# Optimization experiments

Measured on AMD Instinct MI355X. Metric: run time of the kernel, lower is better.

Reference implementation:

```python
import jax, jax.numpy as jnp
import numpy as np


def setup_inputs() -> dict:
    key = jax.random.key(0)
    k1, k2, k3, k4, k5, k6 = jax.random.split(key, 6)
    B, T, K = 64, 1024, 256
    inputs = jax.random.normal(k1, (B, T, K), dtype=jnp.float32)
    tags = jax.random.randint(k2, (B, T), 0, K, dtype=jnp.int64)
    mask = jnp.ones((B, T), dtype=jnp.int32)
    # xavier_normal-ish std for [K,K]: sqrt(2/(K+K))
    transitions = jax.random.normal(k3, (K, K), dtype=jnp.float32) * np.float32(np.sqrt(1.0 / K))
    start_transitions = jax.random.normal(k4, (K,), dtype=jnp.float32)
    end_transitions = jax.random.normal(k5, (K,), dtype=jnp.float32)
    return {
        "inputs": inputs,
        "tags": tags,
        "mask": mask,
        "transitions": transitions,
        "start_transitions": start_transitions,
        "end_transitions": end_transitions,
    }


def _crf_log_likelihood(inputs, tags, mask, transitions, start_transitions, end_transitions):
    # inputs: [B,T,K] emission logits; tags/mask: [B,T]
    B, T, K = inputs.shape
    logits = jnp.transpose(inputs, (1, 0, 2))      # [T,B,K]
    tags_t = tags.T                                 # [T,B]
    maskf = mask.T.astype(inputs.dtype)             # [T,B]
    lengths = jnp.sum(mask, axis=1)                 # [B]
    end_idx = lengths - 1                           # last valid timestep per batch

    # ---- numerator: score of the gold path ----
    # potentials[t,b,i,j] = logits[t,b,i] + transitions[j,i]; gold path picks
    # (i=tags[t], j=tags[t-1]); t=0 picks column 0 = logits[0]+start.
    emit = jnp.take_along_axis(logits, tags_t[:, :, None], axis=2)[..., 0]  # [T,B]
    trans_sc = transitions[tags_t[:-1], tags_t[1:]]                          # [T-1,B]
    last_tags = tags_t[end_idx, jnp.arange(B)]                               # [B]
    numerator = (emit[0]
                 + start_transitions[tags_t[0]]
                 + jnp.sum(maskf[1:] * (emit[1:] + trans_sc), axis=0)
                 + end_transitions[last_tags])                               # [B]

    # ---- denominator: forward algorithm (log-sum-exp over all paths) ----
    is_end = (jnp.arange(T)[:, None] == end_idx[None, :]).astype(inputs.dtype)  # [T,B]
    alpha0 = logits[0] + start_transitions[None, :] + is_end[0][:, None] * end_transitions[None, :]

    def step(alpha, xs):
        lg, m, ie = xs  # lg: [B,K], m/ie: [B]
        # alpha_new[b,i] = logsumexp_j(alpha[b,j] + transitions[j,i]) + logits[t,b,i]
        new = jax.nn.logsumexp(alpha[:, :, None] + transitions[None, :, :], axis=1)
        new = new + lg + ie[:, None] * end_transitions[None, :]
        alpha = jnp.where(m[:, None] > 0, new, alpha)
        return alpha, None

    alphaT, _ = jax.lax.scan(step, alpha0, (logits[1:], maskf[1:], is_end[1:]))
    denominator = jax.nn.logsumexp(alphaT, axis=1)  # [B]

    return jnp.sum(numerator - denominator)


def reference(inputs, tags, mask, transitions, start_transitions, end_transitions):
    return _crf_log_likelihood(inputs, tags, mask, transitions, start_transitions, end_transitions)
```

## Files before the change

kernel.cpp:

```cpp
#include <hip/hip_runtime.h>
#include <hip/hip_fp16.h>

namespace {
constexpr int Bn = 64;
constexpr int Tn = 1024;
constexpr int Kn = 256;
constexpr int TH = 512;

constexpr float LOG2E  = 1.4426950408889634f;
constexpr float LN2    = 0.6931471805599453f;
constexpr float RBIAS  = 4.0f;
constexpr float PCLAMP = 15.5f;

typedef _Float16 half8 __attribute__((ext_vector_type(8)));
typedef float f32x4 __attribute__((ext_vector_type(4)));

__device__ __forceinline__ float fexp2(float x) {
    float r; asm("v_exp_f32 %0, %1" : "=v"(r) : "v"(x)); return r;
}
__device__ __forceinline__ float flog2(float x) {
    float r; asm("v_log_f32 %0, %1" : "=v"(r) : "v"(x)); return r;
}

template <int C>
__device__ __forceinline__ float dppmax1(float x) {
    int o = __builtin_bit_cast(int, x);
    int y = __builtin_amdgcn_update_dpp(o, o, C, 0xF, 0xF, false);
    return fmaxf(x, __builtin_bit_cast(float, y));
}
template <int C>
__device__ __forceinline__ float dppadd1(float x) {
    int y = __builtin_amdgcn_update_dpp(0, __builtin_bit_cast(int, x), C, 0xF, 0xF, true);
    return x + __builtin_bit_cast(float, y);
}
__device__ __forceinline__ float wave_max64(float x) {
    x = dppmax1<0x111>(x);
    x = dppmax1<0x112>(x);
    x = dppmax1<0x114>(x);
    x = dppmax1<0x118>(x);
    x = dppmax1<0x142>(x);
    x = dppmax1<0x143>(x);
    return __builtin_bit_cast(float,
        __builtin_amdgcn_readlane(__builtin_bit_cast(int, x), 63));
}
__device__ __forceinline__ float wave_sum64(float x) {
    x = dppadd1<0x111>(x);
    x = dppadd1<0x112>(x);
    x = dppadd1<0x114>(x);
    x = dppadd1<0x118>(x);
    x = dppadd1<0x142>(x);
    x = dppadd1<0x143>(x);
    return __builtin_bit_cast(float,
        __builtin_amdgcn_readlane(__builtin_bit_cast(int, x), 63));
}
__device__ __forceinline__ float tree4(const f32x4 m) {
    return fmaxf(fmaxf(m[0], m[1]), fmaxf(m[2], m[3]));
}

__global__ __launch_bounds__(256) void efrag_kernel(
    const float* __restrict__ trans, _Float16* __restrict__ efrag)
{
    const int g   = blockIdx.x * 256 + threadIdx.x;
    const int dir = g >> 13;
    const int gg  = g & 8191;
    const int l   = gg & 63;
    const int kt  = (gg >> 6) & 7;
    const int c   = (gg >> 9) & 3;
    const int wg  = (gg >> 11) & 3;
    const int n   = 64 * wg + 16 * c + (l & 15);
    const int k0  = 32 * kt + (l >> 4) * 8;
    half8 hb;
#pragma unroll
    for (int i = 0; i < 8; ++i) {
        const int k = k0 + i;
        hb[i] = (_Float16)__expf(dir == 0 ? trans[k * Kn + n]
                                          : trans[n * Kn + k]);
    }
    ((half8*)efrag)[g] = hb;
}

#define MFMA32_SELECT()                                                          \
    const half8* prow = (const half8*)(&p_sh[PB][0]);                            \
    half8 af0 = prow[0 * 4 + La], af1 = prow[1 * 4 + La];                        \
    half8 af2 = prow[2 * 4 + La], af3 = prow[3 * 4 + La];                        \
    half8 af4 = prow[4 * 4 + La], af5 = prow[5 * 4 + La];                        \
    half8 af6 = prow[6 * 4 + La], af7 = prow[7 * 4 + La];                        \
    f32x4 a0 = __builtin_amdgcn_mfma_f32_16x16x32_f16(af0, Bfrag[0][0], zacc, 0, 0, 0); \
    f32x4 a1 = __builtin_amdgcn_mfma_f32_16x16x32_f16(af0, Bfrag[1][0], zacc, 0, 0, 0); \
    f32x4 a2 = __builtin_amdgcn_mfma_f32_16x16x32_f16(af0, Bfrag[2][0], zacc, 0, 0, 0); \
    f32x4 a3 = __builtin_amdgcn_mfma_f32_16x16x32_f16(af0, Bfrag[3][0], zacc, 0, 0, 0); \
    a0 = __builtin_amdgcn_mfma_f32_16x16x32_f16(af1, Bfrag[0][1], a0, 0, 0, 0);  \
    a1 = __builtin_amdgcn_mfma_f32_16x16x32_f16(af1, Bfrag[1][1], a1, 0, 0, 0);  \
    a2 = __builtin_amdgcn_mfma_f32_16x16x32_f16(af1, Bfrag[2][1], a2, 0, 0, 0);  \
    a3 = __builtin_amdgcn_mfma_f32_16x16x32_f16(af1, Bfrag[3][1], a3, 0, 0, 0);  \
    a0 = __builtin_amdgcn_mfma_f32_16x16x32_f16(af2, Bfrag[0][2], a0, 0, 0, 0);  \
    a1 = __builtin_amdgcn_mfma_f32_16x16x32_f16(af2, Bfrag[1][2], a1, 0, 0, 0);  \
    a2 = __builtin_amdgcn_mfma_f32_16x16x32_f16(af2, Bfrag[2][2], a2, 0, 0, 0);  \
    a3 = __builtin_amdgcn_mfma_f32_16x16x32_f16(af2, Bfrag[3][2], a3, 0, 0, 0);  \
    a0 = __builtin_amdgcn_mfma_f32_16x16x32_f16(af3, Bfrag[0][3], a0, 0, 0, 0);  \
    a1 = __builtin_amdgcn_mfma_f32_16x16x32_f16(af3, Bfrag[1][3], a1, 0, 0, 0);  \
    a2 = __builtin_amdgcn_mfma_f32_16x16x32_f16(af3, Bfrag[2][3], a2, 0, 0, 0);  \
    a3 = __builtin_amdgcn_mfma_f32_16x16x32_f16(af3, Bfrag[3][3], a3, 0, 0, 0);  \
    a0 = __builtin_amdgcn_mfma_f32_16x16x32_f16(af4, Bfrag[0][4], a0, 0, 0, 0);  \
    a1 = __builtin_amdgcn_mfma_f32_16x16x32_f16(af4, Bfrag[1][4], a1, 0, 0, 0);  \
    a2 = __builtin_amdgcn_mfma_f32_16x16x32_f16(af4, Bfrag[2][4], a2, 0, 0, 0);  \
    a3 = __builtin_amdgcn_mfma_f32_16x16x32_f16(af4, Bfrag[3][4], a3, 0, 0, 0);  \
    a0 = __builtin_amdgcn_mfma_f32_16x16x32_f16(af5, Bfrag[0][5], a0, 0, 0, 0);  \
    a1 = __builtin_amdgcn_mfma_f32_16x16x32_f16(af5, Bfrag[1][5], a1, 0, 0, 0);  \
    a2 = __builtin_amdgcn_mfma_f32_16x16x32_f16(af5, Bfrag[2][5], a2, 0, 0, 0);  \
    a3 = __builtin_amdgcn_mfma_f32_16x16x32_f16(af5, Bfrag[3][5], a3, 0, 0, 0);  \
    a0 = __builtin_amdgcn_mfma_f32_16x16x32_f16(af6, Bfrag[0][6], a0, 0, 0, 0);  \
    a1 = __builtin_amdgcn_mfma_f32_16x16x32_f16(af6, Bfrag[1][6], a1, 0, 0, 0);  \
    a2 = __builtin_amdgcn_mfma_f32_16x16x32_f16(af6, Bfrag[2][6], a2, 0, 0, 0);  \
    a3 = __builtin_amdgcn_mfma_f32_16x16x32_f16(af6, Bfrag[3][6], a3, 0, 0, 0);  \
    a0 = __builtin_amdgcn_mfma_f32_16x16x32_f16(af7, Bfrag[0][7], a0, 0, 0, 0);  \
    a1 = __builtin_amdgcn_mfma_f32_16x16x32_f16(af7, Bfrag[1][7], a1, 0, 0, 0);  \
    a2 = __builtin_amdgcn_mfma_f32_16x16x32_f16(af7, Bfrag[2][7], a2, 0, 0, 0);  \
    a3 = __builtin_amdgcn_mfma_f32_16x16x32_f16(af7, Bfrag[3][7], a3, 0, 0, 0);  \
    const float s01 = (La & 1) ? a1[0] : a0[0];                                  \
    const float s23 = (La & 1) ? a3[0] : a2[0];                                  \
    const float s   = (La & 2) ? s23 : s01;

template <int PB, int NB>
__device__ __forceinline__ void fwd_step(
    int tcur, float& alpha, float& R_prev,
    float& lg1, float& lg2, float& lg3,
    const float* __restrict__ in_b, int j_own, int La, int wg,
    const half8 (&Bfrag)[4][8], const f32x4 zacc,
    _Float16 (*__restrict__ p_sh)[Kn], float (*__restrict__ Mv)[4])
{
    const float lgC = lg1; lg1 = lg2; lg2 = lg3;
    lg3 = in_b[(size_t)(tcur + 3) * Kn + j_own];
    const float early = fmaf(lgC, LOG2E, R_prev);

    asm volatile("s_waitcnt lgkmcnt(0)" ::: "memory");
    __builtin_amdgcn_s_barrier();
    __builtin_amdgcn_sched_barrier(0);

    const f32x4 mv = *(const f32x4*)(&Mv[NB][0]);
    const float wmx = wave_max64(alpha);
    Mv[PB][wg] = wmx;
    const float R_use = tree4(mv) + RBIAS;

    MFMA32_SELECT()

    alpha = early + flog2(s);
    const float pv = fexp2(fminf(alpha - R_use, PCLAMP));
    p_sh[NB][j_own] = (_Float16)pv;
    R_prev = R_use;
}

template <int PB, int NB>
__device__ __forceinline__ void bwd_step(
    int tcur, float& beta, float& x, float& R_prev,
    float& lg1, float& lg2, float& lg3,
    const float* __restrict__ in_b, int j_own, int La, int wg,
    const half8 (&Bfrag)[4][8], const f32x4 zacc,
    _Float16 (*__restrict__ p_sh)[Kn], float (*__restrict__ Mv)[4])
{
    const float lgC = lg1; lg1 = lg2; lg2 = lg3;
    lg3 = in_b[(size_t)(tcur - 3) * Kn + j_own];
    const float lgC2 = lgC * LOG2E;

    asm volatile("s_waitcnt lgkmcnt(0)" ::: "memory");
    __builtin_amdgcn_s_barrier();
    __builtin_amdgcn_sched_barrier(0);

    const f32x4 mv = *(const f32x4*)(&Mv[NB][0]);
    const float wmx = wave_max64(x);
    Mv[PB][wg] = wmx;
    const float R_use = tree4(mv) + RBIAS;

    MFMA32_SELECT()

    beta = R_prev + flog2(s);
    x = beta + lgC2;
    const float qv = fexp2(fminf(x - R_use, PCLAMP));
    p_sh[NB][j_own] = (_Float16)qv;
    R_prev = R_use;
}

template <int PB, int NB>
__device__ __forceinline__ void m_step(
    int tcur, float& alpha, float& R_prev,
    float& lg1, float& lg2, float& lg3,
    const float* __restrict__ in_b, int j_own, int La, int wg,
    const half8 (&Bfrag)[4][8], const f32x4 zacc,
    _Float16 (*__restrict__ p_sh)[Kn], float (*__restrict__ Mv)[4],
    const int* __restrict__ mask_sh)
{
    const float lgC = lg1; lg1 = lg2; lg2 = lg3;
    const int tp3 = (tcur + 3 < Tn) ? (tcur + 3) : (Tn - 1);
    lg3 = in_b[(size_t)tp3 * Kn + j_own];
    const int mkC = mask_sh[tcur];

    asm volatile("s_waitcnt lgkmcnt(0)" ::: "memory");
    __builtin_amdgcn_s_barrier();
    __builtin_amdgcn_sched_barrier(0);

    const f32x4 mv = *(const f32x4*)(&Mv[NB][0]);
    const float wmx = wave_max64(alpha);
    Mv[PB][wg] = wmx;
    const float R_use = tree4(mv) + RBIAS;

    MFMA32_SELECT()

    const float na = R_prev + flog2(s) + lgC * LOG2E;
    if (mkC > 0) alpha = na;
    const float pv = fexp2(fminf(alpha - R_use, PCLAMP));
    p_sh[NB][j_own] = (_Float16)pv;
    R_prev = R_use;
}

__global__ __launch_bounds__(256, 1) void crf_main(
    const float* __restrict__ inputs,
    const long long* __restrict__ tags,
    const int* __restrict__ mask,
    const _Float16* __restrict__ efrag,
    const float* __restrict__ trans,
    const float* __restrict__ start_t,
    const float* __restrict__ end_t,
    float* __restrict__ out,
    float* __restrict__ aw,
    float* __restrict__ bw)
{
    const int bid = blockIdx.x;
    const int b   = bid >> 1;
    const int dir = bid & 1;
    const int tid = threadIdx.x;
    const int wg  = tid >> 6;
    const int l   = tid & 63;
    const int La  = l >> 4;
    const int j_own = 64 * wg + l;

    __shared__ __align__(16) _Float16 p_sh[2][Kn];
    __shared__ __align__(16) float Mv[2][4];
    __shared__ int   mask_sh[Tn];
    __shared__ float sh_np;
    __shared__ int   sh_len;

    if (tid == 0) { sh_len = 0; sh_np = 0.f; }

    int cnt = 0;
    for (int t = tid; t < Tn; t += 256) {
        const int m = mask[b * Tn + t];
        mask_sh[t] = m;
        cnt += (m > 0) ? 1 : 0;
    }
    __syncthreads();
    {
        const float cf = wave_sum64((float)cnt);
        if (l == 0) atomicAdd(&sh_len, (int)(cf + 0.5f));
    }

    half8 Bfrag[4][8];
    if (efrag != nullptr) {
        const half8* ef = (const half8*)efrag;
        const int base = dir * 8192;
#pragma unroll
        for (int c = 0; c < 4; ++c)
#pragma unroll
            for (int kt = 0; kt < 8; ++kt)
                Bfrag[c][kt] = ef[base + ((wg * 4 + c) * 8 + kt) * 64 + l];
    } else {
#pragma unroll
        for (int c = 0; c < 4; ++c) {
            const int n = 64 * wg + 16 * c + (l & 15);
#pragma unroll
            for (int kt = 0; kt < 8; ++kt) {
                const int k0 = 32 * kt + La * 8;
                half8 hb;
#pragma unroll
                for (int i = 0; i < 8; ++i) {
                    const int k = k0 + i;
                    hb[i] = (_Float16)__expf(dir == 0 ? trans[k * Kn + n]
                                                      : trans[n * Kn + k]);
                }
                Bfrag[c][kt] = hb;
            }
        }
    }

    const size_t bTK = (size_t)b * (size_t)(Tn * Kn);
    const float* in_b = inputs + bTK;
    const float endj  = end_t[j_own];

    f32x4 zacc = {0.f, 0.f, 0.f, 0.f};
    asm volatile("" : "+v"(zacc));

    float alpha = 0.f, beta = 0.f, x = 0.f;
    float lg1 = 0.f, lg2 = 0.f, lg3 = 0.f;
    if (dir == 0) {
        alpha = (in_b[j_own] + start_t[j_own]) * LOG2E;
        lg1 = in_b[1 * Kn + j_own];
        lg2 = in_b[2 * Kn + j_own];
        lg3 = in_b[3 * Kn + j_own];
        Mv[1][wg] = wave_max64(alpha);
    } else {
        beta = endj * LOG2E;
        x    = beta + in_b[(size_t)(Tn - 1) * Kn + j_own] * LOG2E;
        lg1 = in_b[(size_t)(Tn - 2) * Kn + j_own];
        lg2 = in_b[(size_t)(Tn - 3) * Kn + j_own];
        lg3 = in_b[(size_t)(Tn - 4) * Kn + j_own];
        Mv[1][wg] = wave_max64(x);
    }
    __syncthreads();
    const int end_idx = sh_len - 1;

    float R_prev;
    {
        R_prev = tree4(*(const f32x4*)(&Mv[1][0])) + RBIAS;
        const float v0 = (dir == 0) ? alpha : x;
        const float pv = fexp2(fminf(v0 - R_prev, PCLAMP));
        p_sh[0][j_own] = (_Float16)pv;
    }

    if (sh_len == Tn) {
        if (dir == 0) {
            for (int t = 1; t <= TH; t += 2) {
                fwd_step<0, 1>(t,     alpha, R_prev, lg1, lg2, lg3,
                               in_b, j_own, La, wg, Bfrag, zacc, p_sh, Mv);
                fwd_step<1, 0>(t + 1, alpha, R_prev, lg1, lg2, lg3,
                               in_b, j_own, La, wg, Bfrag, zacc, p_sh, Mv);
            }
            aw[b * Kn + j_own] = alpha;
        } else {
            bwd_step<0, 1>(1022, beta, x, R_prev, lg1, lg2, lg3,
                           in_b, j_own, La, wg, Bfrag, zacc, p_sh, Mv);
            for (int t = 1021; t >= 513; t -= 2) {
                bwd_step<1, 0>(t,     beta, x, R_prev, lg1, lg2, lg3,
                               in_b, j_own, La, wg, Bfrag, zacc, p_sh, Mv);
                bwd_step<0, 1>(t - 1, beta, x, R_prev, lg1, lg2, lg3,
                               in_b, j_own, La, wg, Bfrag, zacc, p_sh, Mv);
            }
            bw[b * Kn + j_own] = beta;
        }
    } else {
        if (dir == 0) {
            m_step<0, 1>(1, alpha, R_prev, lg1, lg2, lg3, in_b, j_own, La, wg,
                         Bfrag, zacc, p_sh, Mv, mask_sh);
            for (int t = 2; t < Tn; t += 2) {
                m_step<1, 0>(t,     alpha, R_prev, lg1, lg2, lg3, in_b, j_own, La,
                             wg, Bfrag, zacc, p_sh, Mv, mask_sh);
                m_step<0, 1>(t + 1, alpha, R_prev, lg1, lg2, lg3, in_b, j_own, La,
                             wg, Bfrag, zacc, p_sh, Mv, mask_sh);
            }
            aw[b * Kn + j_own] = alpha + endj * LOG2E;
        } else {
            bw[b * Kn + tid] = 0.f;
            return;
        }
    }

    if (dir == 0) {
        float np = 0.f;
        for (int t = tid; t < Tn; t += 256) {
            const int   tg = (int)tags[b * Tn + t];
            const float e  = in_b[(size_t)t * Kn + tg];
            if (t == 0) {
                np += e + start_t[tg];
            } else {
                const float mf = (float)mask_sh[t];
                const int   tq = (int)tags[b * Tn + t - 1];
                np += mf * (e + trans[tq * Kn + tg]);
            }
        }
        np = wave_sum64(np);
        if (l == 0) atomicAdd(&sh_np, np);
        __syncthreads();
        if (tid == 0) {
            atomicAdd(out, sh_np + end_t[(int)tags[b * Tn + end_idx]]);
        }
    }
}

__global__ __launch_bounds__(64) void merge_kernel(
    const float* __restrict__ aw, const float* __restrict__ bw,
    float* __restrict__ out)
{
    const int b = blockIdx.x;
    const int l = threadIdx.x;
    const f32x4 va = *(const f32x4*)(aw + b * Kn + 4 * l);
    const f32x4 vb = *(const f32x4*)(bw + b * Kn + 4 * l);
    const float v0 = va[0] + vb[0];
    const float v1 = va[1] + vb[1];
    const float v2 = va[2] + vb[2];
    const float v3 = va[3] + vb[3];
    float m = fmaxf(fmaxf(v0, v1), fmaxf(v2, v3));
    m = wave_max64(m);
    float S = fexp2(v0 - m) + fexp2(v1 - m) + fexp2(v2 - m) + fexp2(v3 - m);
    S = wave_sum64(S);
    if (l == 0) atomicAdd(out, -(LN2 * (m + flog2(S))));
}

}

extern "C" void kernel_launch(void* const* d_in, const int* in_sizes, int n_in,
                              void* d_out, int out_size, void* d_ws, size_t ws_size,
                              hipStream_t stream) {
    const float*     inputs  = (const float*)d_in[0];
    const long long* tags    = (const long long*)d_in[1];
    const int*       mask    = (const int*)d_in[2];
    const float*     trans   = (const float*)d_in[3];
    const float*     start_t = (const float*)d_in[4];
    const float*     end_t   = (const float*)d_in[5];
    float* out = (float*)d_out;

    float*    aw = (float*)d_ws;
    float*    bw = aw + Bn * Kn;
    _Float16* ef = (_Float16*)(bw + Bn * Kn);
    const size_t need_vec = (size_t)2 * Bn * Kn * sizeof(float);
    const size_t need_ef  = need_vec + (size_t)2 * Kn * Kn * sizeof(_Float16);
    const bool useEf = (d_ws != nullptr) && (ws_size >= need_ef);

    (void)hipMemsetAsync(out, 0, sizeof(float), stream);
    if (useEf) {
        efrag_kernel<<<dim3((2 * Kn * Kn / 8) / 256), dim3(256), 0, stream>>>(
            trans, ef);
    }
    crf_main<<<dim3(2 * Bn), dim3(256), 0, stream>>>(
        inputs, tags, mask, useEf ? (const _Float16*)ef : nullptr,
        trans, start_t, end_t, out, aw, bw);
    merge_kernel<<<dim3(Bn), dim3(64), 0, stream>>>(aw, bw, out);
}
```

Before: 335.9 us.

## Move log/max off the recurrence critical path in the forward/backward CRF steps

The forward and backward full-length steps are merged into one templated fast_step. The next probability is now built in linear space as s * exp2(emission) * exp2(R_prev - R_use), so the log2 and exp2 no longer sit between the MFMA result and the LDS store. The log-domain value and its wave max are computed one step late from saved state, taking the max reduction off the dependency chain, with the final alpha/beta rebuilt after the loop. The cost is an extra exp per step, a one-step-stale rescale max, and a saturation clamp of 60000 instead of the exponent clamp, which could lose precision in fp16.

Result: faster. 317.7 us (-5.4%).

```diff
diff --git a/kernel.cpp b/kernel.cpp
--- a/kernel.cpp
+++ b/kernel.cpp
@@ -11,6 +11,7 @@
 constexpr float LN2    = 0.6931471805599453f;
 constexpr float RBIAS  = 4.0f;
 constexpr float PCLAMP = 15.5f;
+constexpr float VCLAMP = 60000.f;
 
 typedef _Float16 half8 __attribute__((ext_vector_type(8)));
 typedef float f32x4 __attribute__((ext_vector_type(4)));
@@ -121,62 +122,39 @@
     const float s23 = (La & 1) ? a3[0] : a2[0];                                  \
     const float s   = (La & 2) ? s23 : s01;
 
-template <int PB, int NB>
-__device__ __forceinline__ void fwd_step(
-    int tcur, float& alpha, float& R_prev,
+template <int PB, int NB, bool FWD>
+__device__ __forceinline__ void fast_step(
+    int tcur, float& R_prev, float& sR, float& s_save, float& em_save,
     float& lg1, float& lg2, float& lg3,
     const float* __restrict__ in_b, int j_own, int La, int wg,
     const half8 (&Bfrag)[4][8], const f32x4 zacc,
     _Float16 (*__restrict__ p_sh)[Kn], float (*__restrict__ Mv)[4])
 {
-    const float lgC = lg1; lg1 = lg2; lg2 = lg3;
-    lg3 = in_b[(size_t)(tcur + 3) * Kn + j_own];
-    const float early = fmaf(lgC, LOG2E, R_prev);
+    const float em_C = lg1 * LOG2E;
+    const float pe_C = fexp2(em_C);
+    lg1 = lg2; lg2 = lg3;
+    lg3 = in_b[(size_t)(FWD ? (tcur + 3) : (tcur - 3)) * Kn + j_own];
 
     asm volatile("s_waitcnt lgkmcnt(0)" ::: "memory");
     __builtin_amdgcn_s_barrier();
     __builtin_amdgcn_sched_barrier(0);
 
     const f32x4 mv = *(const f32x4*)(&Mv[NB][0]);
-    const float wmx = wave_max64(alpha);
-    Mv[PB][wg] = wmx;
     const float R_use = tree4(mv) + RBIAS;
+    const float sc2 = fexp2(R_prev - R_use);
 
     MFMA32_SELECT()
 
-    alpha = early + flog2(s);
-    const float pv = fexp2(fminf(alpha - R_use, PCLAMP));
+    {
+        const float v_prev = sR + flog2(s_save) + em_save;
+        const float wmx = wave_max64(v_prev);
+        Mv[PB][wg] = wmx;
+    }
+
+    const float pv = fminf(s * pe_C * sc2, VCLAMP);
     p_sh[NB][j_own] = (_Float16)pv;
-    R_prev = R_use;
-}
-
-template <int PB, int NB>
-__device__ __forceinline__ void bwd_step(
-    int tcur, float& beta, float& x, float& R_prev,
-    float& lg1, float& lg2, float& lg3,
-    const float* __restrict__ in_b, int j_own, int La, int wg,
-    const half8 (&Bfrag)[4][8], const f32x4 zacc,
-    _Float16 (*__restrict__ p_sh)[Kn], float (*__restrict__ Mv)[4])
-{
-    const float lgC = lg1; lg1 = lg2; lg2 = lg3;
-    lg3 = in_b[(size_t)(tcur - 3) * Kn + j_own];
-    const float lgC2 = lgC * LOG2E;
-
-    asm volatile("s_waitcnt lgkmcnt(0)" ::: "memory");
-    __builtin_amdgcn_s_barrier();
-    __builtin_amdgcn_sched_barrier(0);
-
-    const f32x4 mv = *(const f32x4*)(&Mv[NB][0]);
-    const float wmx = wave_max64(x);
-    Mv[PB][wg] = wmx;
-    const float R_use = tree4(mv) + RBIAS;
-
-    MFMA32_SELECT()
-
-    beta = R_prev + flog2(s);
-    x = beta + lgC2;
-    const float qv = fexp2(fminf(x - R_use, PCLAMP));
-    p_sh[NB][j_own] = (_Float16)qv;
+
+    sR = R_prev; s_save = s; em_save = em_C;
     R_prev = R_use;
 }
 
@@ -288,55 +266,59 @@
     f32x4 zacc = {0.f, 0.f, 0.f, 0.f};
     asm volatile("" : "+v"(zacc));
 
-    float alpha = 0.f, beta = 0.f, x = 0.f;
+    float v0 = 0.f;
     float lg1 = 0.f, lg2 = 0.f, lg3 = 0.f;
     if (dir == 0) {
-        alpha = (in_b[j_own] + start_t[j_own]) * LOG2E;
+        v0  = (in_b[j_own] + start_t[j_own]) * LOG2E;
         lg1 = in_b[1 * Kn + j_own];
         lg2 = in_b[2 * Kn + j_own];
         lg3 = in_b[3 * Kn + j_own];
-        Mv[1][wg] = wave_max64(alpha);
     } else {
-        beta = endj * LOG2E;
-        x    = beta + in_b[(size_t)(Tn - 1) * Kn + j_own] * LOG2E;
+        v0  = endj * LOG2E + in_b[(size_t)(Tn - 1) * Kn + j_own] * LOG2E;
         lg1 = in_b[(size_t)(Tn - 2) * Kn + j_own];
         lg2 = in_b[(size_t)(Tn - 3) * Kn + j_own];
         lg3 = in_b[(size_t)(Tn - 4) * Kn + j_own];
-        Mv[1][wg] = wave_max64(x);
-    }
+    }
+    Mv[1][wg] = wave_max64(v0);
     __syncthreads();
     const int end_idx = sh_len - 1;
 
     float R_prev;
     {
         R_prev = tree4(*(const f32x4*)(&Mv[1][0])) + RBIAS;
-        const float v0 = (dir == 0) ? alpha : x;
         const float pv = fexp2(fminf(v0 - R_prev, PCLAMP));
         p_sh[0][j_own] = (_Float16)pv;
     }
 
     if (sh_len == Tn) {
+        float sR = v0, s_save = 1.0f, em_save = 0.0f;
         if (dir == 0) {
             for (int t = 1; t <= TH; t += 2) {
-                fwd_step<0, 1>(t,     alpha, R_prev, lg1, lg2, lg3,
-                               in_b, j_own, La, wg, Bfrag, zacc, p_sh, Mv);
-                fwd_step<1, 0>(t + 1, alpha, R_prev, lg1, lg2, lg3,
-                               in_b, j_own, La, wg, Bfrag, zacc, p_sh, Mv);
+                fast_step<0, 1, true>(t,     R_prev, sR, s_save, em_save,
+                                      lg1, lg2, lg3, in_b, j_own, La, wg,
+                                      Bfrag, zacc, p_sh, Mv);
+                fast_step<1, 0, true>(t + 1, R_prev, sR, s_save, em_save,
+                                      lg1, lg2, lg3, in_b, j_own, La, wg,
+                                      Bfrag, zacc, p_sh, Mv);
             }
-            aw[b * Kn + j_own] = alpha;
+            aw[b * Kn + j_own] = sR + flog2(s_save) + em_save;
         } else {
-            bwd_step<0, 1>(1022, beta, x, R_prev, lg1, lg2, lg3,
-                           in_b, j_own, La, wg, Bfrag, zacc, p_sh, Mv);
+            fast_step<0, 1, false>(1022, R_prev, sR, s_save, em_save,
+                                   lg1, lg2, lg3, in_b, j_own, La, wg,
+                                   Bfrag, zacc, p_sh, Mv);
             for (int t = 1021; t >= 513; t -= 2) {
-                bwd_step<1, 0>(t,     beta, x, R_prev, lg1, lg2, lg3,
-                               in_b, j_own, La, wg, Bfrag, zacc, p_sh, Mv);
-                bwd_step<0, 1>(t - 1, beta, x, R_prev, lg1, lg2, lg3,
-                               in_b, j_own, La, wg, Bfrag, zacc, p_sh, Mv);
+                fast_step<1, 0, false>(t,     R_prev, sR, s_save, em_save,
+                                       lg1, lg2, lg3, in_b, j_own, La, wg,
+                                       Bfrag, zacc, p_sh, Mv);
+                fast_step<0, 1, false>(t - 1, R_prev, sR, s_save, em_save,
+                                       lg1, lg2, lg3, in_b, j_own, La, wg,
+                                       Bfrag, zacc, p_sh, Mv);
             }
-            bw[b * Kn + j_own] = beta;
+            bw[b * Kn + j_own] = sR + flog2(s_save);
         }
     } else {
         if (dir == 0) {
+            float alpha = v0;
             m_step<0, 1>(1, alpha, R_prev, lg1, lg2, lg3, in_b, j_own, La, wg,
                          Bfrag, zacc, p_sh, Mv, mask_sh);
             for (int t = 2; t < Tn; t += 2) {
```
